# Kernel tuning notes

Measured on AMD Instinct MI355X. Metric: run time of the kernel, lower is better.

The kernel has to match this reference:

```python
import jax, jax.numpy as jnp
import numpy as np

N, F_IN, H1, H2, E = 100000, 256, 128, 64, 1600000


def _glorot(key, shape):
    lim = np.sqrt(6.0 / (shape[0] + shape[1]))
    return jax.random.uniform(key, shape, jnp.float32, -lim, lim)


def setup_inputs() -> dict:
    key = jax.random.key(0)
    ks = jax.random.split(key, 8)
    x = jax.random.normal(ks[0], (N, F_IN), jnp.float32)
    edge_index = jax.random.randint(ks[1], (2, E), 0, N, jnp.int64)
    return {
        "x": x,
        "w1": _glorot(ks[2], (F_IN, H1)),
        "b1": jnp.zeros((H1,), jnp.float32),
        "w2": _glorot(ks[3], (H1, H2)),
        "b2": jnp.zeros((H2,), jnp.float32),
        "w3": _glorot(ks[4], (H1, H2)),
        "b3": jnp.zeros((H2,), jnp.float32),
        "edge_index": edge_index,
    }


def _gcn_conv(x, w, b, src, dst, dinv_sqrt):
    # GCNConv: transform first, then symmetric-normalized aggregation with self-loops.
    h = x @ w                                   # [N, out]
    coef = dinv_sqrt[src] * dinv_sqrt[dst]      # [E]
    agg = jnp.zeros_like(h).at[dst].add(h[src] * coef[:, None])
    # self-loop contribution: coefficient deg^-1 per node
    agg = agg + h * (dinv_sqrt * dinv_sqrt)[:, None]
    return agg + b


def reference(x, w1, b1, w2, b2, w3, b3, edge_index):
    src, dst = edge_index[0], edge_index[1]
    n = x.shape[0]
    # degree including self-loop (edge weights all 1)
    deg = jnp.ones((n,), x.dtype).at[dst].add(1.0)
    dinv_sqrt = jax.lax.rsqrt(deg)
    hidden = jax.nn.relu(_gcn_conv(x, w1, b1, src, dst, dinv_sqrt))
    mu = _gcn_conv(hidden, w2, b2, src, dst, dinv_sqrt)
    logvar = _gcn_conv(hidden, w3, b3, src, dst, dinv_sqrt)
    return (mu, logvar)
```

## Files before the change

### kernel.cpp

```cpp
#include <hip/hip_runtime.h>


#define TPB 256
#define GSHIFT 9
#define GSIZE 512
#define PART_M 8192

typedef __attribute__((ext_vector_type(8))) short short8;
typedef __attribute__((ext_vector_type(4))) short short4v;
typedef __attribute__((ext_vector_type(4))) float floatx4;

__device__ __forceinline__ void split2(float v, short& hi, short& lo) {
    unsigned u = __float_as_uint(v);
    float hf = __uint_as_float(u & 0xFFFF0000u);
    float lf = v - hf;
    hi = (short)(u >> 16);
    lo = (short)(__float_as_uint(lf) >> 16);
}

__device__ __forceinline__ short bf16_rtn(float v) {
    unsigned u = __float_as_uint(v);
    u += 0x7FFF + ((u >> 16) & 1);
    return (short)(u >> 16);
}

__device__ __forceinline__ void addrow(float* a, uint4 v) {
    a[0] += __uint_as_float(v.x << 16); a[1] += __uint_as_float(v.x & 0xFFFF0000u);
    a[2] += __uint_as_float(v.y << 16); a[3] += __uint_as_float(v.y & 0xFFFF0000u);
    a[4] += __uint_as_float(v.z << 16); a[5] += __uint_as_float(v.z & 0xFFFF0000u);
    a[6] += __uint_as_float(v.w << 16); a[7] += __uint_as_float(v.w & 0xFFFF0000u);
}

__global__ __launch_bounds__(TPB) void group_count(const int* __restrict__ dst,
                                                   int* __restrict__ ghist, int E) {
    __shared__ int h[256];
    int t = threadIdx.x;
    h[t] = 0;
    __syncthreads();
    int stride = gridDim.x * TPB;
    for (int k = blockIdx.x * TPB + t; k < E; k += stride)
        atomicAdd(&h[dst[k] >> GSHIFT], 1);
    __syncthreads();
    if (h[t]) atomicAdd(&ghist[t], h[t]);
}

__global__ __launch_bounds__(256) void goff_scan(const int* __restrict__ ghist,
                                                 int* __restrict__ goff, int ngrp) {
    __shared__ int sc[256];
    int t = threadIdx.x;
    int v = (t < ngrp) ? ghist[t] : 0;
    sc[t] = v;
    __syncthreads();
#pragma unroll
    for (int off = 1; off < 256; off <<= 1) {
        int x = (t >= off) ? sc[t - off] : 0;
        __syncthreads();
        sc[t] += x;
        __syncthreads();
    }
    goff[t] = sc[t] - v;
    if (t == 255) goff[256] = sc[255];
}

__global__ __launch_bounds__(256) void partition_kernel(const int* __restrict__ src,
                                                        const int* __restrict__ dst,
                                                        const int* __restrict__ goff,
                                                        int* __restrict__ gcur,
                                                        int* __restrict__ staged, int E) {
    __shared__ int sorted[PART_M];
    __shared__ int sc[256];
    __shared__ int lstart[257];
    __shared__ int cur[256];
    __shared__ int gb[256];
    int t = threadIdx.x;
    int base = blockIdx.x * PART_M;
    int mloc = min(PART_M, E - base);

    sc[t] = 0;
    cur[t] = 0;
    __syncthreads();
    for (int k = t; k < mloc; k += 256)
        atomicAdd(&sc[dst[base + k] >> GSHIFT], 1);
    __syncthreads();
    int v = sc[t];
    __syncthreads();
    sc[t] = v;
    __syncthreads();
#pragma unroll
    for (int off = 1; off < 256; off <<= 1) {
        int x = (t >= off) ? sc[t - off] : 0;
        __syncthreads();
        sc[t] += x;
        __syncthreads();
    }
    lstart[t] = sc[t] - v;
    if (t == 255) lstart[256] = sc[255];
    gb[t] = goff[t] + atomicAdd(&gcur[t], v);
    __syncthreads();
    for (int k = t; k < mloc; k += 256) {
        int d = dst[base + k];
        int s = src[base + k];
        int b = d >> GSHIFT;
        int pos = lstart[b] + atomicAdd(&cur[b], 1);
        sorted[pos] = (s << GSHIFT) | (d & (GSIZE - 1));
    }
    __syncthreads();
    for (int e = t; e < mloc; e += 256) {
        int lo = 0, hi = 256;
        while (hi - lo > 1) {
            int mid = (lo + hi) >> 1;
            if (lstart[mid] <= e) lo = mid; else hi = mid;
        }
        staged[gb[lo] + (e - lstart[lo])] = sorted[e];
    }
}

__global__ __launch_bounds__(512) void build_csr(const int* __restrict__ staged,
                                                 const int* __restrict__ goff,
                                                 int* __restrict__ cnt,
                                                 float* __restrict__ dinv,
                                                 int* __restrict__ rowptr,
                                                 int* __restrict__ csr, int N) {
    __shared__ int hist[512];
    __shared__ int sc[512];
    __shared__ int lrow[512];
    __shared__ int cur[512];
    int t = threadIdx.x;
    int g = blockIdx.x;
    int s0 = goff[g], s1 = goff[g + 1];
    hist[t] = 0;
    cur[t] = 0;
    __syncthreads();
    for (int k = s0 + t; k < s1; k += 512)
        atomicAdd(&hist[staged[k] & (GSIZE - 1)], 1);
    __syncthreads();
    int v = hist[t];
    sc[t] = v;
    __syncthreads();
#pragma unroll
    for (int off = 1; off < 512; off <<= 1) {
        int x = (t >= off) ? sc[t - off] : 0;
        __syncthreads();
        sc[t] += x;
        __syncthreads();
    }
    int rp = s0 + sc[t] - v;
    lrow[t] = rp;
    int node = (g << GSHIFT) + t;
    if (node < N) {
        rowptr[node] = rp;
        cnt[node] = v;
        dinv[node] = rsqrtf(1.0f + (float)v);
    }
    __syncthreads();
    for (int k = s0 + t; k < s1; k += 512) {
        int p = staged[k];
        int dl = p & (GSIZE - 1);
        int pos = lrow[dl] + atomicAdd(&cur[dl], 1);
        csr[pos] = p >> GSHIFT;
    }
}

__global__ void prep_w1t(const float* __restrict__ w1, short* __restrict__ th,
                         short* __restrict__ tl) {
    int t = blockIdx.x * TPB + threadIdx.x;
    int k = t & 255, n = t >> 8;
    float v = w1[(size_t)k * 128 + n];
    short h, l;
    split2(v, h, l);
    th[t] = h;
    tl[t] = l;
}

__global__ void prep_wcatt(const float* __restrict__ w2, const float* __restrict__ b2,
                           const float* __restrict__ w3, const float* __restrict__ b3,
                           short* __restrict__ th, short* __restrict__ tl,
                           float* __restrict__ bcat) {
    int t = blockIdx.x * TPB + threadIdx.x;
    int k = t & 127, n = t >> 7;
    float v = (n < 64) ? w2[(size_t)k * 64 + n] : w3[(size_t)k * 64 + (n - 64)];
    short h, l;
    split2(v, h, l);
    th[t] = h;
    tl[t] = l;
    if (t < 64) { bcat[t] = b2[t]; bcat[64 + t] = b3[t]; }
}

__global__ __launch_bounds__(TPB) void gemm_mfma_f32in(const float* __restrict__ A,
                                                       const short* __restrict__ Bth,
                                                       const short* __restrict__ Btl,
                                                       const float* __restrict__ rs,
                                                       short* __restrict__ Cb, int M, int K) {
    __shared__ short Ah[4 * 64 * 8], Al[4 * 64 * 8];
    __shared__ short Bh[4 * 128 * 8], Bl[4 * 128 * 8];
    int t = threadIdx.x;
    int wave = t >> 6, lane = t & 63, quad = lane >> 4, l16 = lane & 15;
    int bm0 = blockIdx.x * 64;

    floatx4 acc[8];
#pragma unroll
    for (int nt = 0; nt < 8; ++nt) acc[nt] = (floatx4){0.f, 0.f, 0.f, 0.f};

    for (int k0 = 0; k0 < K; k0 += 32) {
#pragma unroll
        for (int i = 0; i < 2; ++i) {
            int c = t + i * 256;
            int row = c >> 3;
            int kc = (c & 7) * 4;
            int gr = bm0 + row;
            float4 v = (gr < M) ? *(const float4*)(A + (size_t)gr * K + k0 + kc)
                                : make_float4(0.f, 0.f, 0.f, 0.f);
            short h0, l0, h1, l1, h2, l2, h3, l3;
            split2(v.x, h0, l0);
            split2(v.y, h1, l1);
            split2(v.z, h2, l2);
            split2(v.w, h3, l3);
            int base = ((kc >> 3) * 64 + row) * 8 + (kc & 7);
            *(short4v*)&Ah[base] = (short4v){h0, h1, h2, h3};
            *(short4v*)&Al[base] = (short4v){l0, l1, l2, l3};
        }
#pragma unroll
        for (int i = 0; i < 2; ++i) {
            int c = t + i * 256;
            int n = c >> 2, kq = c & 3;
            size_t g = (size_t)n * K + k0 + kq * 8;
            int base = (kq * 128 + n) * 8;
            *(short8*)&Bh[base] = *(const short8*)(Bth + g);
            *(short8*)&Bl[base] = *(const short8*)(Btl + g);
        }
        __syncthreads();
        int am = wave * 16 + l16;
        short8 a_h = *(const short8*)&Ah[(quad * 64 + am) * 8];
        short8 a_l = *(const short8*)&Al[(quad * 64 + am) * 8];
#pragma unroll
        for (int nt = 0; nt < 8; ++nt) {
            int bn = nt * 16 + l16;
            short8 b_h = *(const short8*)&Bh[(quad * 128 + bn) * 8];
            short8 b_l = *(const short8*)&Bl[(quad * 128 + bn) * 8];
            acc[nt] = __builtin_amdgcn_mfma_f32_16x16x32_bf16(a_l, b_h, acc[nt], 0, 0, 0);
            acc[nt] = __builtin_amdgcn_mfma_f32_16x16x32_bf16(a_h, b_l, acc[nt], 0, 0, 0);
            acc[nt] = __builtin_amdgcn_mfma_f32_16x16x32_bf16(a_h, b_h, acc[nt], 0, 0, 0);
        }
        __syncthreads();
    }
#pragma unroll
    for (int reg = 0; reg < 4; ++reg) {
        int gr = bm0 + wave * 16 + quad * 4 + reg;
        if (gr < M) {
            float s = rs[gr];
            short* cp = Cb + (size_t)gr * 128;
#pragma unroll
            for (int nt = 0; nt < 8; ++nt) cp[nt * 16 + l16] = bf16_rtn(acc[nt][reg] * s);
        }
    }
}

__global__ __launch_bounds__(TPB) void gemm_mfma_bfin(const short* __restrict__ AH,
                                                      const short* __restrict__ AL,
                                                      const short* __restrict__ Bth,
                                                      const short* __restrict__ Btl,
                                                      const float* __restrict__ rs,
                                                      short* __restrict__ Cb, int M, int K) {
    __shared__ short Ah[4 * 64 * 8], Al[4 * 64 * 8];
    __shared__ short Bh[4 * 128 * 8], Bl[4 * 128 * 8];
    int t = threadIdx.x;
    int wave = t >> 6, lane = t & 63, quad = lane >> 4, l16 = lane & 15;
    int bm0 = blockIdx.x * 64;

    floatx4 acc[8];
#pragma unroll
    for (int nt = 0; nt < 8; ++nt) acc[nt] = (floatx4){0.f, 0.f, 0.f, 0.f};

    for (int k0 = 0; k0 < K; k0 += 32) {
        {
            int row = t >> 2, kc = (t & 3) * 8;
            int gr = bm0 + row;
            uint4 vh = make_uint4(0u, 0u, 0u, 0u), vl = vh;
            if (gr < M) {
                size_t g = (size_t)gr * K + k0 + kc;
                vh = *(const uint4*)(AH + g);
                vl = *(const uint4*)(AL + g);
            }
            int base = ((kc >> 3) * 64 + row) * 8;
            *(uint4*)&Ah[base] = vh;
            *(uint4*)&Al[base] = vl;
        }
#pragma unroll
        for (int i = 0; i < 2; ++i) {
            int c = t + i * 256;
            int n = c >> 2, kq = c & 3;
            size_t g = (size_t)n * K + k0 + kq * 8;
            int base = (kq * 128 + n) * 8;
            *(short8*)&Bh[base] = *(const short8*)(Bth + g);
            *(short8*)&Bl[base] = *(const short8*)(Btl + g);
        }
        __syncthreads();
        int am = wave * 16 + l16;
        short8 a_h = *(const short8*)&Ah[(quad * 64 + am) * 8];
        short8 a_l = *(const short8*)&Al[(quad * 64 + am) * 8];
#pragma unroll
        for (int nt = 0; nt < 8; ++nt) {
            int bn = nt * 16 + l16;
            short8 b_h = *(const short8*)&Bh[(quad * 128 + bn) * 8];
            short8 b_l = *(const short8*)&Bl[(quad * 128 + bn) * 8];
            acc[nt] = __builtin_amdgcn_mfma_f32_16x16x32_bf16(a_l, b_h, acc[nt], 0, 0, 0);
            acc[nt] = __builtin_amdgcn_mfma_f32_16x16x32_bf16(a_h, b_l, acc[nt], 0, 0, 0);
            acc[nt] = __builtin_amdgcn_mfma_f32_16x16x32_bf16(a_h, b_h, acc[nt], 0, 0, 0);
        }
        __syncthreads();
    }
#pragma unroll
    for (int reg = 0; reg < 4; ++reg) {
        int gr = bm0 + wave * 16 + quad * 4 + reg;
        if (gr < M) {
            float s = rs[gr];
            short* cp = Cb + (size_t)gr * 128;
#pragma unroll
            for (int nt = 0; nt < 8; ++nt) cp[nt * 16 + l16] = bf16_rtn(acc[nt][reg] * s);
        }
    }
}

__global__ __launch_bounds__(TPB) void gather_hidden(const int* __restrict__ csr,
                                                     const int* __restrict__ rowptr,
                                                     const int* __restrict__ cnt,
                                                     const float* __restrict__ dinv,
                                                     const short* __restrict__ hs,
                                                     const float* __restrict__ b1,
                                                     short* __restrict__ hidH,
                                                     short* __restrict__ hidL, int N) {
    size_t t = (size_t)blockIdx.x * TPB + threadIdx.x;
    int nid = (int)(t >> 4);
    int lane = threadIdx.x & 15;
    if (nid >= N) return;
    int start = rowptr[nid];
    int deg = cnt[nid];
    const uint4* hp = (const uint4*)hs;
    float acc[8] = {0, 0, 0, 0, 0, 0, 0, 0};
    addrow(acc, hp[(size_t)nid * 16 + lane]);
    int j = 0;
    for (; j + 1 < deg; j += 2) {
        int s0 = csr[start + j], s1 = csr[start + j + 1];
        uint4 v0 = hp[(size_t)s0 * 16 + lane];
        uint4 v1 = hp[(size_t)s1 * 16 + lane];
        addrow(acc, v0);
        addrow(acc, v1);
    }
    if (j < deg) addrow(acc, hp[(size_t)csr[start + j] * 16 + lane]);
    float di = dinv[nid];
    float4 b0 = ((const float4*)b1)[lane * 2];
    float4 b1v = ((const float4*)b1)[lane * 2 + 1];
    float bb[8] = {b0.x, b0.y, b0.z, b0.w, b1v.x, b1v.y, b1v.z, b1v.w};
    unsigned hiw[8];
    short low[8];
#pragma unroll
    for (int i = 0; i < 8; ++i) {
        float h = fmaxf(fmaf(di, acc[i], bb[i]), 0.f);
        unsigned u = __float_as_uint(h);
        hiw[i] = u >> 16;
        float hf = __uint_as_float(u & 0xFFFF0000u);
        low[i] = bf16_rtn(h - hf);
    }
    uint4 ph, pl;
    ph.x = hiw[0] | (hiw[1] << 16);
    ph.y = hiw[2] | (hiw[3] << 16);
    ph.z = hiw[4] | (hiw[5] << 16);
    ph.w = hiw[6] | (hiw[7] << 16);
    pl.x = (unsigned short)low[0] | ((unsigned)(unsigned short)low[1] << 16);
    pl.y = (unsigned short)low[2] | ((unsigned)(unsigned short)low[3] << 16);
    pl.z = (unsigned short)low[4] | ((unsigned)(unsigned short)low[5] << 16);
    pl.w = (unsigned short)low[6] | ((unsigned)(unsigned short)low[7] << 16);
    ((uint4*)hidH)[(size_t)nid * 16 + lane] = ph;
    ((uint4*)hidL)[(size_t)nid * 16 + lane] = pl;
}

__global__ __launch_bounds__(TPB) void gather_out(const int* __restrict__ csr,
                                                  const int* __restrict__ rowptr,
                                                  const int* __restrict__ cnt,
                                                  const float* __restrict__ dinv,
                                                  const short* __restrict__ hs,
                                                  const float* __restrict__ bcat,
                                                  float* __restrict__ out, int N) {
    size_t t = (size_t)blockIdx.x * TPB + threadIdx.x;
    int nid = (int)(t >> 4);
    int lane = threadIdx.x & 15;
    if (nid >= N) return;
    int start = rowptr[nid];
    int deg = cnt[nid];
    const uint4* hp = (const uint4*)hs;
    float acc[8] = {0, 0, 0, 0, 0, 0, 0, 0};
    addrow(acc, hp[(size_t)nid * 16 + lane]);
    int j = 0;
    for (; j + 1 < deg; j += 2) {
        int s0 = csr[start + j], s1 = csr[start + j + 1];
        uint4 v0 = hp[(size_t)s0 * 16 + lane];
        uint4 v1 = hp[(size_t)s1 * 16 + lane];
        addrow(acc, v0);
        addrow(acc, v1);
    }
    if (j < deg) addrow(acc, hp[(size_t)csr[start + j] * 16 + lane]);
    float di = dinv[nid];
    float4 b0 = ((const float4*)bcat)[lane * 2];
    float4 b1v = ((const float4*)bcat)[lane * 2 + 1];
    float4 r0, r1;
    r0.x = fmaf(di, acc[0], b0.x);
    r0.y = fmaf(di, acc[1], b0.y);
    r0.z = fmaf(di, acc[2], b0.z);
    r0.w = fmaf(di, acc[3], b0.w);
    r1.x = fmaf(di, acc[4], b1v.x);
    r1.y = fmaf(di, acc[5], b1v.y);
    r1.z = fmaf(di, acc[6], b1v.z);
    r1.w = fmaf(di, acc[7], b1v.w);
    int f = lane * 8;
    float* dp = (f < 64) ? (out + (size_t)nid * 64 + f)
                         : (out + (size_t)N * 64 + (size_t)nid * 64 + (f - 64));
    *(float4*)dp = r0;
    *(float4*)(dp + 4) = r1;
}

extern "C" void kernel_launch(void* const* d_in, const int* in_sizes, int n_in,
                              void* d_out, int out_size, void* d_ws, size_t ws_size,
                              hipStream_t stream) {
    const float* x  = (const float*)d_in[0];
    const float* w1 = (const float*)d_in[1];
    const float* b1 = (const float*)d_in[2];
    const float* w2 = (const float*)d_in[3];
    const float* b2 = (const float*)d_in[4];
    const float* w3 = (const float*)d_in[5];
    const float* b3 = (const float*)d_in[6];
    const int*   ei = (const int*)d_in[7];

    const int N = in_sizes[0] / 256;
    const int E = in_sizes[7] / 2;
    const int K1 = 256;

    float* out = (float*)d_out;

    size_t nh = (size_t)N * 128;
    short* hs1    = (short*)d_ws;
    short* hidH   = hs1 + nh;
    short* hidL   = hidH + nh;
    short* hs2    = hidL + nh;
    int*   cnt    = (int*)(hs2 + nh);
    float* dinv   = (float*)(cnt + N);
    int*   rowptr = (int*)(dinv + N);
    int*   cursor = rowptr + N;
    int*   bsum   = cursor + N;
    float* bcat   = (float*)(bsum + 512);
    short* w1t_h  = (short*)(bcat + 128);
    short* w1t_l  = w1t_h + 128 * 256;
    short* wct_h  = w1t_l + 128 * 256;
    short* wct_l  = wct_h + 128 * 128;
    int*   csr    = (int*)(wct_l + 128 * 128);

    const int* srcp = ei;
    const int* dstp = ei + E;

    const int ngrp = (N + GSIZE - 1) >> GSHIFT;
    int* ghist  = cursor;
    int* gcur   = cursor + 256;
    int* goff   = cursor + 512;
    int* staged = (int*)hs2;

    hipMemsetAsync(cursor, 0, 512 * sizeof(int), stream);

    int gc_blocks = (E + TPB * 16 - 1) / (TPB * 16);
    group_count<<<gc_blocks, TPB, 0, stream>>>(dstp, ghist, E);
    goff_scan<<<1, 256, 0, stream>>>(ghist, goff, ngrp);
    partition_kernel<<<(E + PART_M - 1) / PART_M, 256, 0, stream>>>(srcp, dstp, goff, gcur,
                                                                    staged, E);
    build_csr<<<ngrp, 512, 0, stream>>>(staged, goff, cnt, dinv, rowptr, csr, N);

    prep_w1t<<<(128 * 256) / TPB, TPB, 0, stream>>>(w1, w1t_h, w1t_l);
    prep_wcatt<<<(128 * 128) / TPB, TPB, 0, stream>>>(w2, b2, w3, b3, wct_h, wct_l, bcat);

    gemm_mfma_f32in<<<(N + 63) / 64, TPB, 0, stream>>>(x, w1t_h, w1t_l, dinv, hs1, N, K1);

    size_t gthreads = (size_t)N * 16;
    gather_hidden<<<(unsigned)((gthreads + TPB - 1) / TPB), TPB, 0, stream>>>(
        csr, rowptr, cnt, dinv, hs1, b1, hidH, hidL, N);

    gemm_mfma_bfin<<<(N + 63) / 64, TPB, 0, stream>>>(hidH, hidL, wct_h, wct_l, dinv, hs2, N, 128);

    gather_out<<<(unsigned)((gthreads + TPB - 1) / TPB), TPB, 0, stream>>>(
        csr, rowptr, cnt, dinv, hs2, bcat, out, N);
}
```

Before: 452.1 us.

## Double-buffer GEMM tiles via direct global-to-LDS loads with swizzled layout

```diff
diff --git a/kernel.cpp b/kernel.cpp
--- a/kernel.cpp
+++ b/kernel.cpp
@@ -29,6 +29,12 @@
     a[2] += __uint_as_float(v.y << 16); a[3] += __uint_as_float(v.y & 0xFFFF0000u);
     a[4] += __uint_as_float(v.z << 16); a[5] += __uint_as_float(v.z & 0xFFFF0000u);
     a[6] += __uint_as_float(v.w << 16); a[7] += __uint_as_float(v.w & 0xFFFF0000u);
+}
+
+__device__ __forceinline__ void gload_lds16(const void* g, void* l) {
+    __builtin_amdgcn_global_load_lds(
+        (const __attribute__((address_space(1))) unsigned int*)g,
+        (__attribute__((address_space(3))) unsigned int*)l, 16, 0, 0);
 }
 
 __global__ __launch_bounds__(TPB) void group_count(const int* __restrict__ dst,
@@ -191,8 +197,9 @@
                                                        const short* __restrict__ Btl,
                                                        const float* __restrict__ rs,
                                                        short* __restrict__ Cb, int M, int K) {
-    __shared__ short Ah[4 * 64 * 8], Al[4 * 64 * 8];
-    __shared__ short Bh[4 * 128 * 8], Bl[4 * 128 * 8];
+    __shared__ float Af[2][64 * 32];
+    __shared__ short Bh[2][128 * 32];
+    __shared__ short Bl[2][128 * 32];
     int t = threadIdx.x;
     int wave = t >> 6, lane = t & 63, quad = lane >> 4, l16 = lane & 15;
     int bm0 = blockIdx.x * 64;
@@ -201,42 +208,58 @@
 #pragma unroll
     for (int nt = 0; nt < 8; ++nt) acc[nt] = (floatx4){0.f, 0.f, 0.f, 0.f};
 
-    for (int k0 = 0; k0 < K; k0 += 32) {
+    auto stage = [&](int pb, int k0) {
 #pragma unroll
         for (int i = 0; i < 2; ++i) {
-            int c = t + i * 256;
-            int row = c >> 3;
-            int kc = (c & 7) * 4;
+            int g = i * 256 + t;
+            int row = g >> 3, col = g & 7;
             int gr = bm0 + row;
-            float4 v = (gr < M) ? *(const float4*)(A + (size_t)gr * K + k0 + kc)
-                                : make_float4(0.f, 0.f, 0.f, 0.f);
-            short h0, l0, h1, l1, h2, l2, h3, l3;
-            split2(v.x, h0, l0);
-            split2(v.y, h1, l1);
-            split2(v.z, h2, l2);
-            split2(v.w, h3, l3);
-            int base = ((kc >> 3) * 64 + row) * 8 + (kc & 7);
-            *(short4v*)&Ah[base] = (short4v){h0, h1, h2, h3};
-            *(short4v*)&Al[base] = (short4v){l0, l1, l2, l3};
+            if (gr >= M) gr = M - 1;
+            int scol = col ^ (row & 7);
+            gload_lds16(A + (size_t)gr * K + k0 + scol * 4,
+                        &Af[pb][(i * 256 + wave * 64) * 4]);
         }
 #pragma unroll
         for (int i = 0; i < 2; ++i) {
-            int c = t + i * 256;
-            int n = c >> 2, kq = c & 3;
-            size_t g = (size_t)n * K + k0 + kq * 8;
-            int base = (kq * 128 + n) * 8;
-            *(short8*)&Bh[base] = *(const short8*)(Bth + g);
-            *(short8*)&Bl[base] = *(const short8*)(Btl + g);
-        }
-        __syncthreads();
-        int am = wave * 16 + l16;
-        short8 a_h = *(const short8*)&Ah[(quad * 64 + am) * 8];
-        short8 a_l = *(const short8*)&Al[(quad * 64 + am) * 8];
+            int g = i * 256 + t;
+            int row = g >> 2, col = g & 3;
+            int scol = col ^ ((row >> 1) & 3);
+            size_t off = (size_t)row * K + k0 + scol * 8;
+            int lb = (i * 256 + wave * 64) * 8;
+            gload_lds16(Bth + off, &Bh[pb][lb]);
+            gload_lds16(Btl + off, &Bl[pb][lb]);
+        }
+    };
+
+    int nk = K >> 5;
+    stage(0, 0);
+    __syncthreads();
+    int am = wave * 16 + l16;
+    int ac0 = ((quad * 2 + 0) ^ (am & 7)) * 4;
+    int ac1 = ((quad * 2 + 1) ^ (am & 7)) * 4;
+    int bc = (quad ^ ((l16 >> 1) & 3)) * 8;
+    for (int ks = 0; ks < nk; ++ks) {
+        int pb = ks & 1;
+        if (ks + 1 < nk) stage(pb ^ 1, (ks + 1) << 5);
+        float4 fa0 = *(const float4*)&Af[pb][am * 32 + ac0];
+        float4 fa1 = *(const float4*)&Af[pb][am * 32 + ac1];
+        short8 a_h, a_l;
+        {
+            short h, l;
+            split2(fa0.x, h, l); a_h[0] = h; a_l[0] = l;
+            split2(fa0.y, h, l); a_h[1] = h; a_l[1] = l;
+            split2(fa0.z, h, l); a_h[2] = h; a_l[2] = l;
+            split2(fa0.w, h, l); a_h[3] = h; a_l[3] = l;
+            split2(fa1.x, h, l); a_h[4] = h; a_l[4] = l;
+            split2(fa1.y, h, l); a_h[5] = h; a_l[5] = l;
+            split2(fa1.z, h, l); a_h[6] = h; a_l[6] = l;
+            split2(fa1.w, h, l); a_h[7] = h; a_l[7] = l;
+        }
 #pragma unroll
         for (int nt = 0; nt < 8; ++nt) {
             int bn = nt * 16 + l16;
-            short8 b_h = *(const short8*)&Bh[(quad * 128 + bn) * 8];
-            short8 b_l = *(const short8*)&Bl[(quad * 128 + bn) * 8];
+            short8 b_h = *(const short8*)&Bh[pb][bn * 32 + bc];
+            short8 b_l = *(const short8*)&Bl[pb][bn * 32 + bc];
             acc[nt] = __builtin_amdgcn_mfma_f32_16x16x32_bf16(a_l, b_h, acc[nt], 0, 0, 0);
             acc[nt] = __builtin_amdgcn_mfma_f32_16x16x32_bf16(a_h, b_l, acc[nt], 0, 0, 0);
             acc[nt] = __builtin_amdgcn_mfma_f32_16x16x32_bf16(a_h, b_h, acc[nt], 0, 0, 0);
@@ -261,8 +284,8 @@
                                                       const short* __restrict__ Btl,
                                                       const float* __restrict__ rs,
                                                       short* __restrict__ Cb, int M, int K) {
-    __shared__ short Ah[4 * 64 * 8], Al[4 * 64 * 8];
-    __shared__ short Bh[4 * 128 * 8], Bl[4 * 128 * 8];
+    __shared__ short Ah[2][64 * 32], Al[2][64 * 32];
+    __shared__ short Bh[2][128 * 32], Bl[2][128 * 32];
     int t = threadIdx.x;
     int wave = t >> 6, lane = t & 63, quad = lane >> 4, l16 = lane & 15;
     int bm0 = blockIdx.x * 64;
@@ -271,38 +294,45 @@
 #pragma unroll
     for (int nt = 0; nt < 8; ++nt) acc[nt] = (floatx4){0.f, 0.f, 0.f, 0.f};
 
-    for (int k0 = 0; k0 < K; k0 += 32) {
+    auto stage = [&](int pb, int k0) {
         {
-            int row = t >> 2, kc = (t & 3) * 8;
+            int row = t >> 2, col = t & 3;
             int gr = bm0 + row;
-            uint4 vh = make_uint4(0u, 0u, 0u, 0u), vl = vh;
-            if (gr < M) {
-                size_t g = (size_t)gr * K + k0 + kc;
-                vh = *(const uint4*)(AH + g);
-                vl = *(const uint4*)(AL + g);
-            }
-            int base = ((kc >> 3) * 64 + row) * 8;
-            *(uint4*)&Ah[base] = vh;
-            *(uint4*)&Al[base] = vl;
+            if (gr >= M) gr = M - 1;
+            int scol = col ^ ((row >> 1) & 3);
+            size_t off = (size_t)gr * K + k0 + scol * 8;
+            int lb = (wave * 64) * 8;
+            gload_lds16(AH + off, &Ah[pb][lb]);
+            gload_lds16(AL + off, &Al[pb][lb]);
         }
 #pragma unroll
         for (int i = 0; i < 2; ++i) {
-            int c = t + i * 256;
-            int n = c >> 2, kq = c & 3;
-            size_t g = (size_t)n * K + k0 + kq * 8;
-            int base = (kq * 128 + n) * 8;
-            *(short8*)&Bh[base] = *(const short8*)(Bth + g);
-            *(short8*)&Bl[base] = *(const short8*)(Btl + g);
-        }
-        __syncthreads();
-        int am = wave * 16 + l16;
-        short8 a_h = *(const short8*)&Ah[(quad * 64 + am) * 8];
-        short8 a_l = *(const short8*)&Al[(quad * 64 + am) * 8];
+            int g = i * 256 + t;
+            int row = g >> 2, col = g & 3;
+            int scol = col ^ ((row >> 1) & 3);
+            size_t off = (size_t)row * K + k0 + scol * 8;
+            int lb = (i * 256 + wave * 64) * 8;
+            gload_lds16(Bth + off, &Bh[pb][lb]);
+            gload_lds16(Btl + off, &Bl[pb][lb]);
+        }
+    };
+
+    int nk = K >> 5;
+    stage(0, 0);
+    __syncthreads();
+    int am = wave * 16 + l16;
+    int ac = (quad ^ ((am >> 1) & 3)) * 8;
+    int bc = (quad ^ ((l16 >> 1) & 3)) * 8;
+    for (int ks = 0; ks < nk; ++ks) {
+        int pb = ks & 1;
+        if (ks + 1 < nk) stage(pb ^ 1, (ks + 1) << 5);
+        short8 a_h = *(const short8*)&Ah[pb][am * 32 + ac];
+        short8 a_l = *(const short8*)&Al[pb][am * 32 + ac];
 #pragma unroll
         for (int nt = 0; nt < 8; ++nt) {
             int bn = nt * 16 + l16;
-            short8 b_h = *(const short8*)&Bh[(quad * 128 + bn) * 8];
-            short8 b_l = *(const short8*)&Bl[(quad * 128 + bn) * 8];
+            short8 b_h = *(const short8*)&Bh[pb][bn * 32 + bc];
+            short8 b_l = *(const short8*)&Bl[pb][bn * 32 + bc];
             acc[nt] = __builtin_amdgcn_mfma_f32_16x16x32_bf16(a_l, b_h, acc[nt], 0, 0, 0);
             acc[nt] = __builtin_amdgcn_mfma_f32_16x16x32_bf16(a_h, b_l, acc[nt], 0, 0, 0);
             acc[nt] = __builtin_amdgcn_mfma_f32_16x16x32_bf16(a_h, b_h, acc[nt], 0, 0, 0);
```

Measured after the change: 430.1 us. 1.05x faster.
